# Kernel optimization log

Hardware: AMD Instinct MI355X
Metric: run time of the kernel (lower is better)

## Reference

```python
import jax, jax.numpy as jnp
import numpy as np

B, N, C = 4, 4096, 1024
NUM_HEADS = 16
HEAD_DIM = C // NUM_HEADS


def setup_inputs() -> dict:
    key = jax.random.key(0)
    k1, k2, k3, k4 = jax.random.split(key, 4)
    s_in = 1.0 / np.sqrt(C)
    return {
        "x": jax.random.normal(k1, (B, N, C), dtype=jnp.float32),
        "H": 64,
        "W": 64,
        "Wqkv": jax.random.normal(k2, (3 * C, C), dtype=jnp.float32) * s_in,
        "Wproj": jax.random.normal(k3, (C, C), dtype=jnp.float32) * s_in,
        "bproj": jnp.zeros((C,), dtype=jnp.float32),
        "alpha": jnp.ones((NUM_HEADS,), dtype=jnp.float32),
    }


def reference(x, H, W, Wqkv, Wproj, bproj, alpha):
    Bb, Nn, Cc = x.shape
    h, d = NUM_HEADS, HEAD_DIM
    # qkv: [B, N, 3C] -> [3, B, h, N, d]
    qkv = jnp.einsum('bnc,oc->bno', x, Wqkv)
    qkv = qkv.reshape(Bb, Nn, 3, h, d).transpose(2, 0, 3, 1, 4)
    q, k, v = qkv[0], qkv[1], qkv[2]  # each [B, h, N, d]
    # channel attention: contract over tokens N -> [B, h, d, d]
    attn = jnp.einsum('bhnd,bhne->bhde', k, q) / alpha[None, :, None, None]
    attn = jax.nn.softmax(attn, axis=-1)
    # (dropout is identity in eval/reference mode)
    # head_out: [B, h, d, N] -> transpose -> [B, N, h, d] -> concat heads
    out = jnp.einsum('bhde,bhne->bhdn', attn, v)
    out = out.transpose(0, 3, 1, 2).reshape(Bb, Nn, Cc)
    return jnp.einsum('bnc,oc->bno', out, Wproj) + bproj
```

## Files before the change

### kernel.cpp

```cpp
#include <hip/hip_runtime.h>
#include <hip/hip_bf16.h>
#include <cstdint>
#include <cstddef>

typedef unsigned short u16;
typedef __bf16 bf16x8 __attribute__((ext_vector_type(8)));
typedef float f32x4 __attribute__((ext_vector_type(4)));
typedef unsigned short u16x4 __attribute__((ext_vector_type(4)));

#define AS1(p) ((__attribute__((address_space(1))) void*)(p))
#define AS3(p) ((__attribute__((address_space(3))) void*)(p))

__device__ __forceinline__ float bf2f(u16 u) {
  unsigned v = ((unsigned)u) << 16; float f; __builtin_memcpy(&f, &v, 4); return f;
}
__device__ __forceinline__ u16 f2bf(float f) {
  unsigned u; __builtin_memcpy(&u, &f, 4);
  u += 0x7FFFu + ((u >> 16) & 1u);
  return (u16)(u >> 16);
}

__global__ __launch_bounds__(256) void convert_kernel(const float* __restrict__ src,
                                                      u16* __restrict__ dst, int n4) {
  int i = blockIdx.x * blockDim.x + threadIdx.x;
  int stride = gridDim.x * blockDim.x;
  for (; i < n4; i += stride) {
    float4 v = ((const float4*)src)[i];
    u16x4 o;
    o.x = f2bf(v.x); o.y = f2bf(v.y); o.z = f2bf(v.z); o.w = f2bf(v.w);
    ((u16x4*)dst)[i] = o;
  }
}

__global__ __launch_bounds__(256) void convert_split_kernel(const float* __restrict__ src,
                                                            u16* __restrict__ hi,
                                                            u16* __restrict__ lo, int n4) {
  int i = blockIdx.x * blockDim.x + threadIdx.x;
  int stride = gridDim.x * blockDim.x;
  for (; i < n4; i += stride) {
    float4 v = ((const float4*)src)[i];
    u16x4 oh, ol;
    oh.x = f2bf(v.x); ol.x = f2bf(v.x - bf2f(oh.x));
    oh.y = f2bf(v.y); ol.y = f2bf(v.y - bf2f(oh.y));
    oh.z = f2bf(v.z); ol.z = f2bf(v.z - bf2f(oh.z));
    oh.w = f2bf(v.w); ol.w = f2bf(v.w - bf2f(oh.w));
    ((u16x4*)hi)[i] = oh;
    ((u16x4*)lo)[i] = ol;
  }
}

__global__ __launch_bounds__(256) void transpose_split_kernel(const float* __restrict__ x,
                                                              u16* __restrict__ Xb,
                                                              u16* __restrict__ XThi,
                                                              u16* __restrict__ XTlo) {
  __shared__ u16 lhi[64 * 68];
  __shared__ u16 llo[64 * 68];
  const int t  = threadIdx.x;
  const int nT = blockIdx.x, cT = blockIdx.y, b = blockIdx.z;
  const size_t xbase = ((size_t)b * 4096 + nT * 64) * 1024 + cT * 64;
  const int c4 = (t & 15) * 4;
  const int r0 = t >> 4;
#pragma unroll
  for (int j = 0; j < 4; ++j) {
    int r = r0 + j * 16;
    float4 v = *(const float4*)(x + xbase + (size_t)r * 1024 + c4);
    u16x4 hi;
    hi.x = f2bf(v.x); hi.y = f2bf(v.y); hi.z = f2bf(v.z); hi.w = f2bf(v.w);
    *(u16x4*)(Xb + xbase + (size_t)r * 1024 + c4) = hi;
    u16 lo[4];
    lo[0] = f2bf(v.x - bf2f(hi.x)); lo[1] = f2bf(v.y - bf2f(hi.y));
    lo[2] = f2bf(v.z - bf2f(hi.z)); lo[3] = f2bf(v.w - bf2f(hi.w));
    u16 hia[4] = { hi.x, hi.y, hi.z, hi.w };
#pragma unroll
    for (int i = 0; i < 4; ++i) {
      lhi[(c4 + i) * 68 + r] = hia[i];
      llo[(c4 + i) * 68 + r] = lo[i];
    }
  }
  __syncthreads();
  const int c  = t >> 2;
  const int n0 = (t & 3) * 16;
  const size_t tbase = ((size_t)b * 1024 + cT * 64 + c) * 4096 + nT * 64 + n0;
#pragma unroll
  for (int q = 0; q < 4; ++q) {
    *(u16x4*)(XThi + tbase + q * 4) = *(const u16x4*)(lhi + c * 68 + n0 + q * 4);
    *(u16x4*)(XTlo + tbase + q * 4) = *(const u16x4*)(llo + c * 68 + n0 + q * 4);
  }
}

template<bool OUT_BF16, bool HAS_BIAS>
__global__ __launch_bounds__(256) void gemm_bt(const u16* __restrict__ A,
                                               const u16* __restrict__ B,
                                               void* __restrict__ Cv,
                                               const float* __restrict__ bias,
                                               int M, int N, int K) {
  __shared__ __align__(16) u16 lA[128 * 32];
  __shared__ __align__(16) u16 lB[128 * 32];
  const int tid  = threadIdx.x;
  const int lane = tid & 63;
  const int wave = tid >> 6;
  const int rowTile = blockIdx.x * 128;
  const int colTile = blockIdx.y * 128;
  const int wr = (wave >> 1) * 64;
  const int wc = (wave & 1) * 64;

  f32x4 acc[4][4] = {};
  const int m  = lane & 15;
  const int ko = (lane >> 4) * 8;

  for (int kt = 0; kt < K; kt += 32) {
#pragma unroll
    for (int i = 0; i < 2; ++i) {
      int idx = i * 256 + tid;
      int row = idx >> 2;
      int kc  = (idx & 3) * 8;
      int ldsOff = (i * 256 + (tid & 192)) * 16;
      __builtin_amdgcn_global_load_lds(AS1(A + (size_t)(rowTile + row) * K + kt + kc),
                                       AS3((char*)lA + ldsOff), 16, 0, 0);
      __builtin_amdgcn_global_load_lds(AS1(B + (size_t)(colTile + row) * K + kt + kc),
                                       AS3((char*)lB + ldsOff), 16, 0, 0);
    }
    __syncthreads();
    bf16x8 af[4], bfr[4];
#pragma unroll
    for (int rb = 0; rb < 4; ++rb)
      af[rb] = *(const bf16x8*)(lA + (wr + rb * 16 + m) * 32 + ko);
#pragma unroll
    for (int cb = 0; cb < 4; ++cb)
      bfr[cb] = *(const bf16x8*)(lB + (wc + cb * 16 + m) * 32 + ko);
#pragma unroll
    for (int rb = 0; rb < 4; ++rb)
#pragma unroll
      for (int cb = 0; cb < 4; ++cb)
        acc[rb][cb] = __builtin_amdgcn_mfma_f32_16x16x32_bf16(af[rb], bfr[cb], acc[rb][cb], 0, 0, 0);
    __syncthreads();
  }

  const int crow0 = rowTile + wr + (lane >> 4) * 4;
  const int ccol0 = colTile + wc + (lane & 15);
#pragma unroll
  for (int rb = 0; rb < 4; ++rb) {
#pragma unroll
    for (int cb = 0; cb < 4; ++cb) {
      int col = ccol0 + cb * 16;
      float bv = HAS_BIAS ? bias[col] : 0.f;
#pragma unroll
      for (int r = 0; r < 4; ++r) {
        int row = crow0 + rb * 16 + r;
        float v = acc[rb][cb][r] + bv;
        if (OUT_BF16) ((u16*)Cv)[(size_t)row * N + col] = f2bf(v);
        else          ((float*)Cv)[(size_t)row * N + col] = v;
      }
    }
  }
}

__global__ __launch_bounds__(256) void gemm_gram(const u16* __restrict__ XThi,
                                                 const u16* __restrict__ XTlo,
                                                 float* __restrict__ Gpart) {
  const int job = blockIdx.x;
  const int b   = blockIdx.y;
  int rt, ct, k0, klen, slice;
  if (job < 112) {
    int p = job >> 2, kq = job & 3;
    int i = 0, rem = p;
    while (rem >= 7 - i) { rem -= 7 - i; ++i; }
    int jj = i + 1 + rem;
    if (kq < 2) { rt = i; ct = jj; } else { rt = jj; ct = i; }
    slice = kq & 1;
    k0 = kq * 1024; klen = 1024;
  } else {
    int dd = (job - 112) >> 1, kh = job & 1;
    rt = ct = dd; slice = kh; k0 = kh * 2048; klen = 2048;
  }
  const int rowTile = rt * 128, colTile = ct * 128;

  __shared__ __align__(16) u16 lAh[128 * 32];
  __shared__ __align__(16) u16 lAl[128 * 32];
  __shared__ __align__(16) u16 lBh[128 * 32];
  __shared__ __align__(16) u16 lBl[128 * 32];
  const int tid  = threadIdx.x;
  const int lane = tid & 63;
  const int wave = tid >> 6;
  const int wr = (wave >> 1) * 64;
  const int wc = (wave & 1) * 64;

  const u16* Ah = XThi + ((size_t)b << 22);
  const u16* Al = XTlo + ((size_t)b << 22);

  f32x4 acc[4][4] = {};
  const int m  = lane & 15;
  const int ko = (lane >> 4) * 8;

  for (int kt = k0; kt < k0 + klen; kt += 32) {
#pragma unroll
    for (int i = 0; i < 2; ++i) {
      int idx = i * 256 + tid;
      int row = idx >> 2;
      int kc  = (idx & 3) * 8;
      int ldsOff = (i * 256 + (tid & 192)) * 16;
      size_t aoff = (size_t)(rowTile + row) * 4096 + kt + kc;
      size_t boff = (size_t)(colTile + row) * 4096 + kt + kc;
      __builtin_amdgcn_global_load_lds(AS1(Ah + aoff), AS3((char*)lAh + ldsOff), 16, 0, 0);
      __builtin_amdgcn_global_load_lds(AS1(Al + aoff), AS3((char*)lAl + ldsOff), 16, 0, 0);
      __builtin_amdgcn_global_load_lds(AS1(Ah + boff), AS3((char*)lBh + ldsOff), 16, 0, 0);
      __builtin_amdgcn_global_load_lds(AS1(Al + boff), AS3((char*)lBl + ldsOff), 16, 0, 0);
    }
    __syncthreads();
    bf16x8 ah[4], al[4], bh[4], bl[4];
#pragma unroll
    for (int rb = 0; rb < 4; ++rb) {
      ah[rb] = *(const bf16x8*)(lAh + (wr + rb * 16 + m) * 32 + ko);
      al[rb] = *(const bf16x8*)(lAl + (wr + rb * 16 + m) * 32 + ko);
    }
#pragma unroll
    for (int cb = 0; cb < 4; ++cb) {
      bh[cb] = *(const bf16x8*)(lBh + (wc + cb * 16 + m) * 32 + ko);
      bl[cb] = *(const bf16x8*)(lBl + (wc + cb * 16 + m) * 32 + ko);
    }
#pragma unroll
    for (int rb = 0; rb < 4; ++rb)
#pragma unroll
      for (int cb = 0; cb < 4; ++cb) {
        acc[rb][cb] = __builtin_amdgcn_mfma_f32_16x16x32_bf16(ah[rb], bh[cb], acc[rb][cb], 0, 0, 0);
        acc[rb][cb] = __builtin_amdgcn_mfma_f32_16x16x32_bf16(ah[rb], bl[cb], acc[rb][cb], 0, 0, 0);
        acc[rb][cb] = __builtin_amdgcn_mfma_f32_16x16x32_bf16(al[rb], bh[cb], acc[rb][cb], 0, 0, 0);
      }
    __syncthreads();
  }

  float* out = Gpart + ((size_t)(slice * 4 + b) << 20);
  const int crow0 = rowTile + wr + (lane >> 4) * 4;
  const int ccol0 = colTile + wc + (lane & 15);
#pragma unroll
  for (int rb = 0; rb < 4; ++rb)
#pragma unroll
    for (int cb = 0; cb < 4; ++cb)
#pragma unroll
      for (int r = 0; r < 4; ++r)
        out[(size_t)(crow0 + rb * 16 + r) * 1024 + ccol0 + cb * 16] = acc[rb][cb][r];
}

__global__ __launch_bounds__(256) void gram_reduce_split(const float* __restrict__ Gp,
                                                         u16* __restrict__ Ghi,
                                                         u16* __restrict__ Glo) {
  const int rt = blockIdx.x, ct = blockIdx.y, b = blockIdx.z;
  const bool diag128 = (rt >> 1) == (ct >> 1);
  const float* s0 = Gp + ((size_t)b << 20);
  const float* s1 = Gp + ((size_t)(4 + b) << 20);
  __shared__ float lT[64 * 68];
  const int t = threadIdx.x;
  const int r = t >> 2;
  const int c16 = (t & 3) * 16;

  if (!diag128) {
    const size_t bb = (size_t)(ct * 64 + r) * 1024 + rt * 64 + c16;
#pragma unroll
    for (int q = 0; q < 4; ++q) {
      float4 v0 = *(const float4*)(s0 + bb + q * 4);
      float4 v1 = *(const float4*)(s1 + bb + q * 4);
      float4 s = { v0.x + v1.x, v0.y + v1.y, v0.z + v1.z, v0.w + v1.w };
      *(float4*)(lT + r * 68 + c16 + q * 4) = s;
    }
    __syncthreads();
  }

  const size_t ab = (size_t)(rt * 64 + r) * 1024 + ct * 64 + c16;
  const size_t ob = ((size_t)b << 20) + ab;
#pragma unroll
  for (int q = 0; q < 4; ++q) {
    float4 v0 = *(const float4*)(s0 + ab + q * 4);
    float4 v1 = *(const float4*)(s1 + ab + q * 4);
    float g[4] = { v0.x + v1.x, v0.y + v1.y, v0.z + v1.z, v0.w + v1.w };
    if (!diag128) {
#pragma unroll
      for (int i = 0; i < 4; ++i) g[i] += lT[(c16 + q * 4 + i) * 68 + r];
    }
    u16x4 oh, ol;
    oh.x = f2bf(g[0]); ol.x = f2bf(g[0] - bf2f(oh.x));
    oh.y = f2bf(g[1]); ol.y = f2bf(g[1] - bf2f(oh.y));
    oh.z = f2bf(g[2]); ol.z = f2bf(g[2] - bf2f(oh.z));
    oh.w = f2bf(g[3]); ol.w = f2bf(g[3] - bf2f(oh.w));
    *(u16x4*)(Ghi + ob + q * 4) = oh;
    *(u16x4*)(Glo + ob + q * 4) = ol;
  }
}

__global__ __launch_bounds__(256) void gemm_tprime(const u16* __restrict__ Wqh,
                                                   const u16* __restrict__ Wql,
                                                   const u16* __restrict__ Ghi,
                                                   const u16* __restrict__ Glo,
                                                   u16* __restrict__ Tph,
                                                   u16* __restrict__ Tpl) {
  __shared__ __align__(16) u16 lAh[128 * 32];
  __shared__ __align__(16) u16 lAl[128 * 32];
  __shared__ __align__(16) u16 lBh[128 * 32];
  __shared__ __align__(16) u16 lBl[128 * 32];
  const int tid  = threadIdx.x;
  const int lane = tid & 63;
  const int wave = tid >> 6;
  const int rowTile = blockIdx.x * 128;
  const int colTile = blockIdx.y * 128;
  const size_t zoff = (size_t)blockIdx.z << 20;
  const int wr = (wave >> 1) * 64;
  const int wc = (wave & 1) * 64;

  f32x4 acc[4][4] = {};
  const int m  = lane & 15;
  const int ko = (lane >> 4) * 8;

  for (int kt = 0; kt < 1024; kt += 32) {
#pragma unroll
    for (int i = 0; i < 2; ++i) {
      int idx = i * 256 + tid;
      int row = idx >> 2;
      int kc  = (idx & 3) * 8;
      int ldsOff = (i * 256 + (tid & 192)) * 16;
      size_t aoff = (size_t)(rowTile + row) * 1024 + kt + kc;
      size_t boff = zoff + (size_t)(colTile + row) * 1024 + kt + kc;
      __builtin_amdgcn_global_load_lds(AS1(Wqh + aoff), AS3((char*)lAh + ldsOff), 16, 0, 0);
      __builtin_amdgcn_global_load_lds(AS1(Wql + aoff), AS3((char*)lAl + ldsOff), 16, 0, 0);
      __builtin_amdgcn_global_load_lds(AS1(Ghi + boff), AS3((char*)lBh + ldsOff), 16, 0, 0);
      __builtin_amdgcn_global_load_lds(AS1(Glo + boff), AS3((char*)lBl + ldsOff), 16, 0, 0);
    }
    __syncthreads();
    bf16x8 ah[4], al[4], bh[4], bl[4];
#pragma unroll
    for (int rb = 0; rb < 4; ++rb) {
      ah[rb] = *(const bf16x8*)(lAh + (wr + rb * 16 + m) * 32 + ko);
      al[rb] = *(const bf16x8*)(lAl + (wr + rb * 16 + m) * 32 + ko);
    }
#pragma unroll
    for (int cb = 0; cb < 4; ++cb) {
      bh[cb] = *(const bf16x8*)(lBh + (wc + cb * 16 + m) * 32 + ko);
      bl[cb] = *(const bf16x8*)(lBl + (wc + cb * 16 + m) * 32 + ko);
    }
#pragma unroll
    for (int rb = 0; rb < 4; ++rb)
#pragma unroll
      for (int cb = 0; cb < 4; ++cb) {
        acc[rb][cb] = __builtin_amdgcn_mfma_f32_16x16x32_bf16(ah[rb], bh[cb], acc[rb][cb], 0, 0, 0);
        acc[rb][cb] = __builtin_amdgcn_mfma_f32_16x16x32_bf16(ah[rb], bl[cb], acc[rb][cb], 0, 0, 0);
        acc[rb][cb] = __builtin_amdgcn_mfma_f32_16x16x32_bf16(al[rb], bh[cb], acc[rb][cb], 0, 0, 0);
      }
    __syncthreads();
  }

  const int crow0 = rowTile + wr + (lane >> 4) * 4;
  const int ccol0 = colTile + wc + (lane & 15);
#pragma unroll
  for (int rb = 0; rb < 4; ++rb)
#pragma unroll
    for (int cb = 0; cb < 4; ++cb)
#pragma unroll
      for (int r = 0; r < 4; ++r) {
        float v = acc[rb][cb][r];
        u16 hi = f2bf(v);
        u16 lo = f2bf(v - bf2f(hi));
        size_t off = zoff + (size_t)(crow0 + rb * 16 + r) * 1024 + ccol0 + cb * 16;
        Tph[off] = hi;
        Tpl[off] = lo;
      }
}

__global__ __launch_bounds__(256) void s_softmax_kernel(const u16* __restrict__ Wqh,
                                                        const u16* __restrict__ Wql,
                                                        const u16* __restrict__ Tph,
                                                        const u16* __restrict__ Tpl,
                                                        const float* __restrict__ alpha,
                                                        u16* __restrict__ attn) {
  const int h = blockIdx.x, b = blockIdx.y;
  const int tid = threadIdx.x, lane = tid & 63, wave = tid >> 6;
  __shared__ __align__(16) u16 lAh[64 * 32];
  __shared__ __align__(16) u16 lAl[64 * 32];
  __shared__ __align__(16) u16 lBh[64 * 32];
  __shared__ __align__(16) u16 lBl[64 * 32];

  const size_t aBase = (size_t)(1024 + h * 64) * 1024;
  const size_t bBase = ((size_t)b << 20) + (size_t)(h * 64) * 1024;

  f32x4 acc[4] = {};
  const int m  = lane & 15;
  const int ko = (lane >> 4) * 8;
  const int srow = tid >> 2;
  const int skc  = (tid & 3) * 8;
  const int ldsOff = (tid & 192) * 16;

  for (int kt = 0; kt < 1024; kt += 32) {
    __builtin_amdgcn_global_load_lds(AS1(Wqh + aBase + (size_t)srow * 1024 + kt + skc),
                                     AS3((char*)lAh + ldsOff), 16, 0, 0);
    __builtin_amdgcn_global_load_lds(AS1(Wql + aBase + (size_t)srow * 1024 + kt + skc),
                                     AS3((char*)lAl + ldsOff), 16, 0, 0);
    __builtin_amdgcn_global_load_lds(AS1(Tph + bBase + (size_t)srow * 1024 + kt + skc),
                                     AS3((char*)lBh + ldsOff), 16, 0, 0);
    __builtin_amdgcn_global_load_lds(AS1(Tpl + bBase + (size_t)srow * 1024 + kt + skc),
                                     AS3((char*)lBl + ldsOff), 16, 0, 0);
    __syncthreads();
    bf16x8 ah = *(const bf16x8*)(lAh + (wave * 16 + m) * 32 + ko);
    bf16x8 al = *(const bf16x8*)(lAl + (wave * 16 + m) * 32 + ko);
#pragma unroll
    for (int cb = 0; cb < 4; ++cb) {
      bf16x8 bh = *(const bf16x8*)(lBh + (cb * 16 + m) * 32 + ko);
      bf16x8 bl = *(const bf16x8*)(lBl + (cb * 16 + m) * 32 + ko);
      acc[cb] = __builtin_amdgcn_mfma_f32_16x16x32_bf16(ah, bh, acc[cb], 0, 0, 0);
      acc[cb] = __builtin_amdgcn_mfma_f32_16x16x32_bf16(ah, bl, acc[cb], 0, 0, 0);
      acc[cb] = __builtin_amdgcn_mfma_f32_16x16x32_bf16(al, bh, acc[cb], 0, 0, 0);
    }
    __syncthreads();
  }

  const float invA = 1.f / alpha[h];
  const int g = lane >> 4;
  const size_t obase = (size_t)(b * 16 + h) * 4096;
#pragma unroll
  for (int r = 0; r < 4; ++r) {
    int d = wave * 16 + g * 4 + r;
    float s[4];
#pragma unroll
    for (int cb = 0; cb < 4; ++cb) s[cb] = acc[cb][r] * invA;
    float mx = fmaxf(fmaxf(s[0], s[1]), fmaxf(s[2], s[3]));
#pragma unroll
    for (int o = 1; o < 16; o <<= 1) mx = fmaxf(mx, __shfl_xor(mx, o, 64));
    float e[4]; float sum = 0.f;
#pragma unroll
    for (int cb = 0; cb < 4; ++cb) { e[cb] = __expf(s[cb] - mx); sum += e[cb]; }
#pragma unroll
    for (int o = 1; o < 16; o <<= 1) sum += __shfl_xor(sum, o, 64);
    float inv = 1.f / sum;
#pragma unroll
    for (int cb = 0; cb < 4; ++cb)
      attn[obase + (size_t)d * 64 + cb * 16 + (lane & 15)] = f2bf(e[cb] * inv);
  }
}

__global__ __launch_bounds__(256) void attnv_kernel(const u16* __restrict__ V,
                                                    const u16* __restrict__ attn,
                                                    u16* __restrict__ outmid) {
  const int tile = blockIdx.x;
  const int h    = blockIdx.y;
  const int tid = threadIdx.x, lane = tid & 63, wave = tid >> 6;
  const int b = (tile * 64) >> 12;
  const int bh = b * 16 + h;
  __shared__ __align__(16) u16 vt[64 * 64];
  __shared__ __align__(16) u16 at[64 * 64];
  const size_t baseV = (size_t)tile * 64 * 1024 + (size_t)h * 64;
#pragma unroll
  for (int i = 0; i < 2; ++i) {
    int idx = i * 256 + tid;
    int tok = idx >> 3;
    int c8  = (idx & 7) * 8;
    int ldsOff = (i * 256 + (tid & 192)) * 16;
    __builtin_amdgcn_global_load_lds(AS1(V + baseV + (size_t)tok * 1024 + c8),
                                     AS3((char*)vt + ldsOff), 16, 0, 0);
    __builtin_amdgcn_global_load_lds(AS1(attn + (size_t)bh * 4096 + idx * 8),
                                     AS3((char*)at + ldsOff), 16, 0, 0);
  }
  __syncthreads();
  const int m  = lane & 15;
  const int ko = (lane >> 4) * 8;
  f32x4 acc[4] = {};
#pragma unroll
  for (int ks = 0; ks < 2; ++ks) {
    bf16x8 a = *(const bf16x8*)(vt + (wave * 16 + m) * 64 + ks * 32 + ko);
#pragma unroll
    for (int cb = 0; cb < 4; ++cb) {
      bf16x8 bb = *(const bf16x8*)(at + (cb * 16 + m) * 64 + ks * 32 + ko);
      acc[cb] = __builtin_amdgcn_mfma_f32_16x16x32_bf16(a, bb, acc[cb], 0, 0, 0);
    }
  }
#pragma unroll
  for (int cb = 0; cb < 4; ++cb) {
    int col = h * 64 + cb * 16 + (lane & 15);
#pragma unroll
    for (int r = 0; r < 4; ++r) {
      int row = tile * 64 + wave * 16 + (lane >> 4) * 4 + r;
      outmid[(size_t)row * 1024 + col] = f2bf(acc[cb][r]);
    }
  }
}

extern "C" void kernel_launch(void* const* d_in, const int* in_sizes, int n_in,
                              void* d_out, int out_size, void* d_ws, size_t ws_size,
                              hipStream_t stream) {
  const float* x     = (const float*)d_in[0];
  const float* Wqkv  = (const float*)d_in[3];
  const float* Wproj = (const float*)d_in[4];
  const float* bproj = (const float*)d_in[5];
  const float* alpha = (const float*)d_in[6];

  char* ws = (char*)d_ws;
  u16*   Xb     = (u16*)ws;
  float* Gpart  = (float*)ws;
  u16*   outmid = (u16*)ws;
  u16*   XThi  = (u16*)(ws + 33554432);
  u16*   attnb = (u16*)(ws + 33554432);
  u16*   XTlo  = (u16*)(ws + 67108864);
  u16*   Ghi   = (u16*)(ws + 67108864);
  u16*   Glo   = (u16*)(ws + 75497472);
  u16*   Tph   = (u16*)(ws + 83886080);
  u16*   Tpl   = (u16*)(ws + 92274688);
  u16*   Wqh   = (u16*)(ws + 100663296);
  u16*   Wql   = (u16*)(ws + 106954752);
  u16*   Vb    = (u16*)(ws + 113246208);
  u16*   Wpb   = (u16*)(ws + 146800640);

  transpose_split_kernel<<<dim3(64, 16, 4), 256, 0, stream>>>(x, Xb, XThi, XTlo);
  convert_split_kernel<<<256, 256, 0, stream>>>(Wqkv, Wqh, Wql, 3145728 / 4);
  convert_kernel<<<128, 256, 0, stream>>>(Wproj, Wpb, 1048576 / 4);
  gemm_bt<true, false><<<dim3(128, 8), 256, 0, stream>>>(
      Xb, Wqh + (size_t)2048 * 1024, Vb, nullptr, 16384, 1024, 1024);
  gemm_gram<<<dim3(128, 4), 256, 0, stream>>>(XThi, XTlo, Gpart);
  gram_reduce_split<<<dim3(16, 16, 4), 256, 0, stream>>>(Gpart, Ghi, Glo);
  gemm_tprime<<<dim3(8, 8, 4), 256, 0, stream>>>(Wqh, Wql, Ghi, Glo, Tph, Tpl);
  s_softmax_kernel<<<dim3(16, 4), 256, 0, stream>>>(Wqh, Wql, Tph, Tpl, alpha, attnb);
  attnv_kernel<<<dim3(256, 16), 256, 0, stream>>>(Vb, attnb, outmid);
  gemm_bt<false, true><<<dim3(128, 8), 256, 0, stream>>>(
      outmid, Wpb, d_out, bproj, 16384, 1024, 1024);
}
```

Before: 451.6 us.

## Fold attention into projection weights and stream-K the Gram GEMM with atomics

Replaces the attn·V kernel plus the output projection GEMM with a per-batch folded matrix M = Wproj·blockdiag(attn^T), built by a small kernel, followed by a single V·M^T GEMM with bias. This removes the outmid intermediate round trip through memory and one full-size GEMM's worth of staging. The Gram GEMM now splits 4608 k-chunks per batch evenly over 512 blocks (stream-K style) and accumulates into a memset buffer with float atomics, so the reduce kernel no longer sums two partial slices and only mirrors the upper triangle. In exchange it adds atomic contention, a memset, and nondeterministic float summation order.

```diff
diff --git a/kernel.cpp b/kernel.cpp
--- a/kernel.cpp
+++ b/kernel.cpp
@@ -155,26 +155,73 @@
   }
 }
 
+__global__ __launch_bounds__(256) void gemm_vm(const u16* __restrict__ V,
+                                               const u16* __restrict__ Mb,
+                                               float* __restrict__ Y,
+                                               const float* __restrict__ bias) {
+  __shared__ __align__(16) u16 lA[128 * 32];
+  __shared__ __align__(16) u16 lB[128 * 32];
+  const int tid  = threadIdx.x;
+  const int lane = tid & 63;
+  const int wave = tid >> 6;
+  const int rowTile = blockIdx.x * 128;
+  const int colTile = blockIdx.y * 128;
+  const int bz = blockIdx.z;
+  const u16* A = V + ((size_t)bz << 22);
+  const u16* B = Mb + ((size_t)bz << 20);
+  float* C = Y + ((size_t)bz << 22);
+  const int wr = (wave >> 1) * 64;
+  const int wc = (wave & 1) * 64;
+
+  f32x4 acc[4][4] = {};
+  const int m  = lane & 15;
+  const int ko = (lane >> 4) * 8;
+
+  for (int kt = 0; kt < 1024; kt += 32) {
+#pragma unroll
+    for (int i = 0; i < 2; ++i) {
+      int idx = i * 256 + tid;
+      int row = idx >> 2;
+      int kc  = (idx & 3) * 8;
+      int ldsOff = (i * 256 + (tid & 192)) * 16;
+      __builtin_amdgcn_global_load_lds(AS1(A + (size_t)(rowTile + row) * 1024 + kt + kc),
+                                       AS3((char*)lA + ldsOff), 16, 0, 0);
+      __builtin_amdgcn_global_load_lds(AS1(B + (size_t)(colTile + row) * 1024 + kt + kc),
+                                       AS3((char*)lB + ldsOff), 16, 0, 0);
+    }
+    __syncthreads();
+    bf16x8 af[4], bfr[4];
+#pragma unroll
+    for (int rb = 0; rb < 4; ++rb)
+      af[rb] = *(const bf16x8*)(lA + (wr + rb * 16 + m) * 32 + ko);
+#pragma unroll
+    for (int cb = 0; cb < 4; ++cb)
+      bfr[cb] = *(const bf16x8*)(lB + (wc + cb * 16 + m) * 32 + ko);
+#pragma unroll
+    for (int rb = 0; rb < 4; ++rb)
+#pragma unroll
+      for (int cb = 0; cb < 4; ++cb)
+        acc[rb][cb] = __builtin_amdgcn_mfma_f32_16x16x32_bf16(af[rb], bfr[cb], acc[rb][cb], 0, 0, 0);
+    __syncthreads();
+  }
+
+  const int crow0 = rowTile + wr + (lane >> 4) * 4;
+  const int ccol0 = colTile + wc + (lane & 15);
+#pragma unroll
+  for (int rb = 0; rb < 4; ++rb)
+#pragma unroll
+    for (int cb = 0; cb < 4; ++cb) {
+      int col = ccol0 + cb * 16;
+      float bv = bias[col];
+#pragma unroll
+      for (int r = 0; r < 4; ++r)
+        C[(size_t)(crow0 + rb * 16 + r) * 1024 + col] = acc[rb][cb][r] + bv;
+    }
+}
+
 __global__ __launch_bounds__(256) void gemm_gram(const u16* __restrict__ XThi,
                                                  const u16* __restrict__ XTlo,
                                                  float* __restrict__ Gpart) {
-  const int job = blockIdx.x;
-  const int b   = blockIdx.y;
-  int rt, ct, k0, klen, slice;
-  if (job < 112) {
-    int p = job >> 2, kq = job & 3;
-    int i = 0, rem = p;
-    while (rem >= 7 - i) { rem -= 7 - i; ++i; }
-    int jj = i + 1 + rem;
-    if (kq < 2) { rt = i; ct = jj; } else { rt = jj; ct = i; }
-    slice = kq & 1;
-    k0 = kq * 1024; klen = 1024;
-  } else {
-    int dd = (job - 112) >> 1, kh = job & 1;
-    rt = ct = dd; slice = kh; k0 = kh * 2048; klen = 2048;
-  }
-  const int rowTile = rt * 128, colTile = ct * 128;
-
   __shared__ __align__(16) u16 lAh[128 * 32];
   __shared__ __align__(16) u16 lAl[128 * 32];
   __shared__ __align__(16) u16 lBh[128 * 32];
@@ -184,84 +231,99 @@
   const int wave = tid >> 6;
   const int wr = (wave >> 1) * 64;
   const int wc = (wave & 1) * 64;
-
-  const u16* Ah = XThi + ((size_t)b << 22);
-  const u16* Al = XTlo + ((size_t)b << 22);
-
-  f32x4 acc[4][4] = {};
   const int m  = lane & 15;
   const int ko = (lane >> 4) * 8;
 
-  for (int kt = k0; kt < k0 + klen; kt += 32) {
-#pragma unroll
-    for (int i = 0; i < 2; ++i) {
-      int idx = i * 256 + tid;
-      int row = idx >> 2;
-      int kc  = (idx & 3) * 8;
-      int ldsOff = (i * 256 + (tid & 192)) * 16;
-      size_t aoff = (size_t)(rowTile + row) * 4096 + kt + kc;
-      size_t boff = (size_t)(colTile + row) * 4096 + kt + kc;
-      __builtin_amdgcn_global_load_lds(AS1(Ah + aoff), AS3((char*)lAh + ldsOff), 16, 0, 0);
-      __builtin_amdgcn_global_load_lds(AS1(Al + aoff), AS3((char*)lAl + ldsOff), 16, 0, 0);
-      __builtin_amdgcn_global_load_lds(AS1(Ah + boff), AS3((char*)lBh + ldsOff), 16, 0, 0);
-      __builtin_amdgcn_global_load_lds(AS1(Al + boff), AS3((char*)lBl + ldsOff), 16, 0, 0);
-    }
-    __syncthreads();
-    bf16x8 ah[4], al[4], bh[4], bl[4];
-#pragma unroll
-    for (int rb = 0; rb < 4; ++rb) {
-      ah[rb] = *(const bf16x8*)(lAh + (wr + rb * 16 + m) * 32 + ko);
-      al[rb] = *(const bf16x8*)(lAl + (wr + rb * 16 + m) * 32 + ko);
-    }
-#pragma unroll
-    for (int cb = 0; cb < 4; ++cb) {
-      bh[cb] = *(const bf16x8*)(lBh + (wc + cb * 16 + m) * 32 + ko);
-      bl[cb] = *(const bf16x8*)(lBl + (wc + cb * 16 + m) * 32 + ko);
-    }
+  const int u0 = blockIdx.x * 36;
+  const int b  = u0 / 4608;
+  int ub   = u0 - b * 4608;
+  int tile = ub >> 7;
+  int koff = ub & 127;
+
+  const u16* Ahp = XThi + ((size_t)b << 22);
+  const u16* Alp = XTlo + ((size_t)b << 22);
+  float* out = Gpart + ((size_t)b << 20);
+
+  int remaining = 36;
+  for (int seg = 0; seg < 2 && remaining > 0; ++seg) {
+    int niter = min(remaining, 128 - koff);
+    int t = tile, rt = 0;
+    while (t >= 8 - rt) { t -= 8 - rt; ++rt; }
+    int ct = rt + t;
+    const int rowTile = rt * 128, colTile = ct * 128;
+
+    f32x4 acc[4][4] = {};
+    const int kend = (koff + niter) * 32;
+    for (int kt = koff * 32; kt < kend; kt += 32) {
+#pragma unroll
+      for (int i = 0; i < 2; ++i) {
+        int idx = i * 256 + tid;
+        int row = idx >> 2;
+        int kc  = (idx & 3) * 8;
+        int ldsOff = (i * 256 + (tid & 192)) * 16;
+        size_t aoff = (size_t)(rowTile + row) * 4096 + kt + kc;
+        size_t boff = (size_t)(colTile + row) * 4096 + kt + kc;
+        __builtin_amdgcn_global_load_lds(AS1(Ahp + aoff), AS3((char*)lAh + ldsOff), 16, 0, 0);
+        __builtin_amdgcn_global_load_lds(AS1(Alp + aoff), AS3((char*)lAl + ldsOff), 16, 0, 0);
+        __builtin_amdgcn_global_load_lds(AS1(Ahp + boff), AS3((char*)lBh + ldsOff), 16, 0, 0);
+        __builtin_amdgcn_global_load_lds(AS1(Alp + boff), AS3((char*)lBl + ldsOff), 16, 0, 0);
+      }
+      __syncthreads();
+      bf16x8 ah[4], al[4], bh[4], bl[4];
+#pragma unroll
+      for (int rb = 0; rb < 4; ++rb) {
+        ah[rb] = *(const bf16x8*)(lAh + (wr + rb * 16 + m) * 32 + ko);
+        al[rb] = *(const bf16x8*)(lAl + (wr + rb * 16 + m) * 32 + ko);
+      }
+#pragma unroll
+      for (int cb = 0; cb < 4; ++cb) {
+        bh[cb] = *(const bf16x8*)(lBh + (wc + cb * 16 + m) * 32 + ko);
+        bl[cb] = *(const bf16x8*)(lBl + (wc + cb * 16 + m) * 32 + ko);
+      }
+#pragma unroll
+      for (int rb = 0; rb < 4; ++rb)
+#pragma unroll
+        for (int cb = 0; cb < 4; ++cb) {
+          acc[rb][cb] = __builtin_amdgcn_mfma_f32_16x16x32_bf16(ah[rb], bh[cb], acc[rb][cb], 0, 0, 0);
+          acc[rb][cb] = __builtin_amdgcn_mfma_f32_16x16x32_bf16(ah[rb], bl[cb], acc[rb][cb], 0, 0, 0);
+          acc[rb][cb] = __builtin_amdgcn_mfma_f32_16x16x32_bf16(al[rb], bh[cb], acc[rb][cb], 0, 0, 0);
+        }
+      __syncthreads();
+    }
+
+    const int crow0 = rowTile + wr + (lane >> 4) * 4;
+    const int ccol0 = colTile + wc + (lane & 15);
 #pragma unroll
     for (int rb = 0; rb < 4; ++rb)
 #pragma unroll
-      for (int cb = 0; cb < 4; ++cb) {
-        acc[rb][cb] = __builtin_amdgcn_mfma_f32_16x16x32_bf16(ah[rb], bh[cb], acc[rb][cb], 0, 0, 0);
-        acc[rb][cb] = __builtin_amdgcn_mfma_f32_16x16x32_bf16(ah[rb], bl[cb], acc[rb][cb], 0, 0, 0);
-        acc[rb][cb] = __builtin_amdgcn_mfma_f32_16x16x32_bf16(al[rb], bh[cb], acc[rb][cb], 0, 0, 0);
-      }
-    __syncthreads();
-  }
-
-  float* out = Gpart + ((size_t)(slice * 4 + b) << 20);
-  const int crow0 = rowTile + wr + (lane >> 4) * 4;
-  const int ccol0 = colTile + wc + (lane & 15);
-#pragma unroll
-  for (int rb = 0; rb < 4; ++rb)
-#pragma unroll
-    for (int cb = 0; cb < 4; ++cb)
-#pragma unroll
-      for (int r = 0; r < 4; ++r)
-        out[(size_t)(crow0 + rb * 16 + r) * 1024 + ccol0 + cb * 16] = acc[rb][cb][r];
+      for (int cb = 0; cb < 4; ++cb)
+#pragma unroll
+        for (int r = 0; r < 4; ++r)
+          atomicAdd(&out[(size_t)(crow0 + rb * 16 + r) * 1024 + ccol0 + cb * 16],
+                    acc[rb][cb][r]);
+
+    remaining -= niter;
+    tile += 1;
+    koff = 0;
+  }
 }
 
 __global__ __launch_bounds__(256) void gram_reduce_split(const float* __restrict__ Gp,
                                                          u16* __restrict__ Ghi,
                                                          u16* __restrict__ Glo) {
   const int rt = blockIdx.x, ct = blockIdx.y, b = blockIdx.z;
-  const bool diag128 = (rt >> 1) == (ct >> 1);
-  const float* s0 = Gp + ((size_t)b << 20);
-  const float* s1 = Gp + ((size_t)(4 + b) << 20);
+  const float* P = Gp + ((size_t)b << 20);
+  const bool mirror = (rt >> 1) > (ct >> 1);
   __shared__ float lT[64 * 68];
   const int t = threadIdx.x;
   const int r = t >> 2;
   const int c16 = (t & 3) * 16;
 
-  if (!diag128) {
+  if (mirror) {
     const size_t bb = (size_t)(ct * 64 + r) * 1024 + rt * 64 + c16;
 #pragma unroll
-    for (int q = 0; q < 4; ++q) {
-      float4 v0 = *(const float4*)(s0 + bb + q * 4);
-      float4 v1 = *(const float4*)(s1 + bb + q * 4);
-      float4 s = { v0.x + v1.x, v0.y + v1.y, v0.z + v1.z, v0.w + v1.w };
-      *(float4*)(lT + r * 68 + c16 + q * 4) = s;
-    }
+    for (int q = 0; q < 4; ++q)
+      *(float4*)(lT + r * 68 + c16 + q * 4) = *(const float4*)(P + bb + q * 4);
     __syncthreads();
   }
 
@@ -269,12 +331,13 @@
   const size_t ob = ((size_t)b << 20) + ab;
 #pragma unroll
   for (int q = 0; q < 4; ++q) {
-    float4 v0 = *(const float4*)(s0 + ab + q * 4);
-    float4 v1 = *(const float4*)(s1 + ab + q * 4);
-    float g[4] = { v0.x + v1.x, v0.y + v1.y, v0.z + v1.z, v0.w + v1.w };
-    if (!diag128) {
-#pragma unroll
-      for (int i = 0; i < 4; ++i) g[i] += lT[(c16 + q * 4 + i) * 68 + r];
+    float g[4];
+    if (mirror) {
+#pragma unroll
+      for (int i = 0; i < 4; ++i) g[i] = lT[(c16 + q * 4 + i) * 68 + r];
+    } else {
+      float4 v = *(const float4*)(P + ab + q * 4);
+      g[0] = v.x; g[1] = v.y; g[2] = v.z; g[3] = v.w;
     }
     u16x4 oh, ol;
     oh.x = f2bf(g[0]); ol.x = f2bf(g[0] - bf2f(oh.x));
@@ -368,7 +431,7 @@
                                                         const u16* __restrict__ Tph,
                                                         const u16* __restrict__ Tpl,
                                                         const float* __restrict__ alpha,
-                                                        u16* __restrict__ attn) {
+                                                        u16* __restrict__ attnT) {
   const int h = blockIdx.x, b = blockIdx.y;
   const int tid = threadIdx.x, lane = tid & 63, wave = tid >> 6;
   __shared__ __align__(16) u16 lAh[64 * 32];
@@ -428,55 +491,66 @@
     for (int o = 1; o < 16; o <<= 1) sum += __shfl_xor(sum, o, 64);
     float inv = 1.f / sum;
 #pragma unroll
-    for (int cb = 0; cb < 4; ++cb)
-      attn[obase + (size_t)d * 64 + cb * 16 + (lane & 15)] = f2bf(e[cb] * inv);
-  }
-}
-
-__global__ __launch_bounds__(256) void attnv_kernel(const u16* __restrict__ V,
-                                                    const u16* __restrict__ attn,
-                                                    u16* __restrict__ outmid) {
-  const int tile = blockIdx.x;
-  const int h    = blockIdx.y;
+    for (int cb = 0; cb < 4; ++cb) {
+      int e_idx = cb * 16 + (lane & 15);
+      attnT[obase + (size_t)e_idx * 64 + d] = f2bf(e[cb] * inv);
+    }
+  }
+}
+
+__global__ __launch_bounds__(256) void m_build_kernel(const u16* __restrict__ Wpb,
+                                                      const u16* __restrict__ attnT,
+                                                      u16* __restrict__ Mb) {
+  const int oT = blockIdx.x, h = blockIdx.y, b = blockIdx.z;
   const int tid = threadIdx.x, lane = tid & 63, wave = tid >> 6;
-  const int b = (tile * 64) >> 12;
+  __shared__ __align__(16) u16 lA[128 * 64];
+  __shared__ __align__(16) u16 lB[64 * 64];
   const int bh = b * 16 + h;
-  __shared__ __align__(16) u16 vt[64 * 64];
-  __shared__ __align__(16) u16 at[64 * 64];
-  const size_t baseV = (size_t)tile * 64 * 1024 + (size_t)h * 64;
+#pragma unroll
+  for (int i = 0; i < 4; ++i) {
+    int idx = i * 256 + tid;
+    int row = idx >> 3;
+    int kc  = (idx & 7) * 8;
+    int ldsOff = (i * 256 + (tid & 192)) * 16;
+    __builtin_amdgcn_global_load_lds(AS1(Wpb + (size_t)(oT * 128 + row) * 1024 + h * 64 + kc),
+                                     AS3((char*)lA + ldsOff), 16, 0, 0);
+  }
 #pragma unroll
   for (int i = 0; i < 2; ++i) {
     int idx = i * 256 + tid;
-    int tok = idx >> 3;
-    int c8  = (idx & 7) * 8;
     int ldsOff = (i * 256 + (tid & 192)) * 16;
-    __builtin_amdgcn_global_load_lds(AS1(V + baseV + (size_t)tok * 1024 + c8),
-                                     AS3((char*)vt + ldsOff), 16, 0, 0);
-    __builtin_amdgcn_global_load_lds(AS1(attn + (size_t)bh * 4096 + idx * 8),
-                                     AS3((char*)at + ldsOff), 16, 0, 0);
+    __builtin_amdgcn_global_load_lds(AS1(attnT + (size_t)bh * 4096 + idx * 8),
+                                     AS3((char*)lB + ldsOff), 16, 0, 0);
   }
   __syncthreads();
   const int m  = lane & 15;
   const int ko = (lane >> 4) * 8;
-  f32x4 acc[4] = {};
+  const int wr = wave * 32;
+  f32x4 acc[2][4] = {};
 #pragma unroll
   for (int ks = 0; ks < 2; ++ks) {
-    bf16x8 a = *(const bf16x8*)(vt + (wave * 16 + m) * 64 + ks * 32 + ko);
+#pragma unroll
+    for (int rb = 0; rb < 2; ++rb) {
+      bf16x8 a = *(const bf16x8*)(lA + (wr + rb * 16 + m) * 64 + ks * 32 + ko);
+#pragma unroll
+      for (int cb = 0; cb < 4; ++cb) {
+        bf16x8 bb = *(const bf16x8*)(lB + (cb * 16 + m) * 64 + ks * 32 + ko);
+        acc[rb][cb] = __builtin_amdgcn_mfma_f32_16x16x32_bf16(a, bb, acc[rb][cb], 0, 0, 0);
+      }
+    }
+  }
+  u16* out = Mb + ((size_t)b << 20);
+#pragma unroll
+  for (int rb = 0; rb < 2; ++rb)
 #pragma unroll
     for (int cb = 0; cb < 4; ++cb) {
-      bf16x8 bb = *(const bf16x8*)(at + (cb * 16 + m) * 64 + ks * 32 + ko);
-      acc[cb] = __builtin_amdgcn_mfma_f32_16x16x32_bf16(a, bb, acc[cb], 0, 0, 0);
-    }
-  }
-#pragma unroll
-  for (int cb = 0; cb < 4; ++cb) {
-    int col = h * 64 + cb * 16 + (lane & 15);
-#pragma unroll
-    for (int r = 0; r < 4; ++r) {
-      int row = tile * 64 + wave * 16 + (lane >> 4) * 4 + r;
-      outmid[(size_t)row * 1024 + col] = f2bf(acc[cb][r]);
-    }
-  }
+      int col = h * 64 + cb * 16 + (lane & 15);
+#pragma unroll
+      for (int r = 0; r < 4; ++r) {
+        int row = oT * 128 + wr + rb * 16 + (lane >> 4) * 4 + r;
+        out[(size_t)row * 1024 + col] = f2bf(acc[rb][cb][r]);
+      }
+    }
 }
 
 extern "C" void kernel_launch(void* const* d_in, const int* in_sizes, int n_in,
@@ -491,9 +565,9 @@
   char* ws = (char*)d_ws;
   u16*   Xb     = (u16*)ws;
   float* Gpart  = (float*)ws;
-  u16*   outmid = (u16*)ws;
-  u16*   XThi  = (u16*)(ws + 33554432);
-  u16*   attnb = (u16*)(ws + 33554432);
+  u16*   Mb     = (u16*)ws;
+  u16*   XThi   = (u16*)(ws + 33554432);
+  u16*   attnTb = (u16*)(ws + 33554432);
   u16*   XTlo  = (u16*)(ws + 67108864);
   u16*   Ghi   = (u16*)(ws + 67108864);
   u16*   Glo   = (u16*)(ws + 75497472);
@@ -509,11 +583,11 @@
   convert_kernel<<<128, 256, 0, stream>>>(Wproj, Wpb, 1048576 / 4);
   gemm_bt<true, false><<<dim3(128, 8), 256, 0, stream>>>(
       Xb, Wqh + (size_t)2048 * 1024, Vb, nullptr, 16384, 1024, 1024);
-  gemm_gram<<<dim3(128, 4), 256, 0, stream>>>(XThi, XTlo, Gpart);
+  hipMemsetAsync(Gpart, 0, (size_t)4 * 1024 * 1024 * 4, stream);
+  gemm_gram<<<512, 256, 0, stream>>>(XThi, XTlo, Gpart);
   gram_reduce_split<<<dim3(16, 16, 4), 256, 0, stream>>>(Gpart, Ghi, Glo);
   gemm_tprime<<<dim3(8, 8, 4), 256, 0, stream>>>(Wqh, Wql, Ghi, Glo, Tph, Tpl);
-  s_softmax_kernel<<<dim3(16, 4), 256, 0, stream>>>(Wqh, Wql, Tph, Tpl, alpha, attnb);
-  attnv_kernel<<<dim3(256, 16), 256, 0, stream>>>(Vb, attnb, outmid);
-  gemm_bt<false, true><<<dim3(128, 8), 256, 0, stream>>>(
-      outmid, Wpb, d_out, bproj, 16384, 1024, 1024);
-}
+  s_softmax_kernel<<<dim3(16, 4), 256, 0, stream>>>(Wqh, Wql, Tph, Tpl, alpha, attnTb);
+  m_build_kernel<<<dim3(8, 16, 4), 256, 0, stream>>>(Wpb, attnTb, Mb);
+  gemm_vm<<<dim3(32, 8, 4), 256, 0, stream>>>(Vb, Mb, (float*)d_out, bproj);
+}
```

After: 458.5 us. Within noise of the previous version (+1.5%).
